# Optimization experiments

Hardware: AMD Instinct MI355X
Metric: run time of the kernel (lower is better)

## Reference

```python
import jax, jax.numpy as jnp
import numpy as np

B, S, D, M = 2, 4096, 128, 64

def _linear_init(key, shape, fan_in):
    bound = 1.0 / np.sqrt(fan_in)
    return jax.random.uniform(key, shape, jnp.float32, -bound, bound)

def setup_inputs() -> dict:
    key = jax.random.key(0)
    ks = jax.random.split(key, 18)
    x = jax.random.normal(ks[0], (B, S, D), jnp.float32)
    context = jax.random.normal(ks[1], (B, S, D), jnp.float32)
    # per-mechanism params (torch Linear semantics: y = x @ W.T + b)
    Wt = _linear_init(ks[2], (M, D, D), D)   # transform weight, laid out [m, in, out]
    bt = _linear_init(ks[3], (M, D), D)
    char = jax.random.normal(ks[4], (M, D), jnp.float32)  # characteristics [1,1,d] per mech
    Wg = _linear_init(ks[5], (M, D), D)      # timing_gate weight (out=1)
    bg = _linear_init(ks[6], (M,), D)
    Wv = _linear_init(ks[7], (M, D), D)      # victory_detector weight (out=1)
    bv = _linear_init(ks[8], (M,), D)
    O = jax.random.normal(ks[9], (M, M), jnp.float32) * 0.02  # overcoming matrix
    # selector: Linear(2D,2D) -> GELU -> Linear(2D,M)
    W1 = _linear_init(ks[10], (2 * D, 2 * D), 2 * D)
    b1 = _linear_init(ks[11], (2 * D,), 2 * D)
    W2 = _linear_init(ks[12], (2 * D, M), 2 * D)
    b2 = _linear_init(ks[13], (M,), 2 * D)
    # integrate: Linear(2D, D)
    Wi = _linear_init(ks[14], (2 * D, D), 2 * D)
    bi = _linear_init(ks[15], (D,), 2 * D)
    return {"x": x, "context": context, "Wt": Wt, "bt": bt, "char": char,
            "Wg": Wg, "bg": bg, "Wv": Wv, "bv": bv, "O": O,
            "W1": W1, "b1": b1, "W2": W2, "b2": b2, "Wi": Wi, "bi": bi}

def reference(x, context, Wt, bt, char, Wg, bg, Wv, bv, O, W1, b1, W2, b2, Wi, bi):
    # selection scores over mechanisms
    sel_in = jnp.concatenate([x, context], axis=-1)          # [b,s,2d]
    h = jax.nn.gelu(sel_in @ W1 + b1, approximate=False)
    selection_scores = jax.nn.softmax(h @ W2 + b2, axis=-1)  # [b,s,m]
    # all 64 mechanism nodes as one batched GEMM
    transformed = jnp.einsum('bsd,mde->bsme', x, Wt) + bt + char   # [b,s,m,d]
    timing = jax.nn.sigmoid(jnp.einsum('bsd,md->bsm', x, Wg) + bg)  # [b,s,m]
    victory = jax.nn.sigmoid(jnp.einsum('bsme,me->bsm', transformed, Wv) + bv)
    outputs = transformed * timing[..., None]                # [b,s,m,d]
    # strategic overcoming modulation: gate = 1 + tanh(scores @ O)
    gates = 1.0 + jnp.tanh(selection_scores @ O)             # [b,s,m]
    selected = jnp.einsum('bsme,bsm->bse', outputs, gates * selection_scores)
    victory_potential = jnp.sum(victory * selection_scores, axis=-1)  # [b,s]
    integrated = jnp.concatenate([x, selected], axis=-1) @ Wi + bi    # [b,s,d]
    return integrated, victory_potential
```

## Files before the change

kernel.cpp:

```cpp
#include <hip/hip_runtime.h>
#include <hip/hip_bf16.h>


typedef __bf16 bf16_t;
typedef __bf16 bf16x8 __attribute__((ext_vector_type(8)));
typedef float  f32x4  __attribute__((ext_vector_type(4)));

#define WS_WTT      0u
#define WS_W1T      2097152u
#define WS_W2T      2228224u
#define WS_OT       2260992u
#define WS_WG       2269184u
#define WS_U        2285568u
#define WS_CVEC     2301952u
#define WS_BCT      2302208u
#define WS_WIT      2318592u
#define WS_W        2384128u
#define WS_SBIAS    4481280u
#define WS_SEL      8675584u

#define VP_OFF 1048576

__device__ __forceinline__ f32x4 mfma16(bf16x8 a, bf16x8 b, f32x4 c) {
  return __builtin_amdgcn_mfma_f32_16x16x32_bf16(a, b, c, 0, 0, 0);
}

__device__ __forceinline__ void gld_lds16(const void* g, void* l) {
  __builtin_amdgcn_global_load_lds(
      (const __attribute__((address_space(1))) void*)g,
      (__attribute__((address_space(3))) void*)l, 16, 0, 0);
}

__device__ __forceinline__ float gelu_exact(float v) {
  return 0.5f * v * (1.0f + erff(v * 0.70710678118654752f));
}
__device__ __forceinline__ float sigmoidf_(float v) {
  return 1.0f / (1.0f + __expf(-v));
}

__global__ __launch_bounds__(256) void kprep(
    const float* __restrict__ Wt, const float* __restrict__ bt,
    const float* __restrict__ ch, const float* __restrict__ Wg,
    const float* __restrict__ Wv, const float* __restrict__ bv,
    const float* __restrict__ O, const float* __restrict__ W1,
    const float* __restrict__ W2, const float* __restrict__ Wi,
    char* __restrict__ ws)
{
  const int bid = blockIdx.x, tid = threadIdx.x;
  if (bid < 64) {
    const int m = bid;
    const float* wtm = Wt + m * 16384;
    bf16_t* wtt = (bf16_t*)(ws + WS_WTT) + m * 16384;
    #pragma unroll
    for (int i = 0; i < 8; ++i) {
      int task = tid + i * 256;
      int d = task >> 4, e0 = (task & 15) * 8;
      float vv[8];
      #pragma unroll
      for (int j = 0; j < 8; ++j) vv[j] = wtm[d * 128 + e0 + j];
      #pragma unroll
      for (int j = 0; j < 8; ++j) {
        int e = e0 + j;
        int q = e * 16 + (d >> 3);
        ((bf16_t*)((char*)wtt + ((q ^ (e & 7)) << 4)))[d & 7] = (bf16_t)vv[j];
      }
    }
    if (tid < 128) {
      const float* wvm = Wv + m * 128;
      float s = 0.f;
      for (int e = 0; e < 128; ++e) s += wtm[tid * 128 + e] * wvm[e];
      ((bf16_t*)(ws + WS_U))[m * 128 + tid] = (bf16_t)s;
    } else if (tid == 128) {
      const float* wvm = Wv + m * 128;
      float s = bv[m];
      for (int e = 0; e < 128; ++e) s += (bt[m * 128 + e] + ch[m * 128 + e]) * wvm[e];
      ((float*)(ws + WS_CVEC))[m] = s;
    }
  } else if (bid < 80) {
    int base = (bid - 64) * 256 + tid;
    int k = base >> 4, c0 = (base & 15) * 16;
    bf16_t* o = (bf16_t*)(ws + WS_W1T);
    #pragma unroll
    for (int j = 0; j < 16; ++j) o[(c0 + j) * 256 + k] = (bf16_t)W1[k * 256 + c0 + j];
  } else if (bid < 82) {
    int base = (bid - 80) * 256 + tid;
    int k = base >> 1, c0 = (base & 1) * 32;
    bf16_t* o = (bf16_t*)(ws + WS_W2T);
    #pragma unroll
    for (int j = 0; j < 32; ++j) o[(c0 + j) * 256 + k] = (bf16_t)W2[k * 64 + c0 + j];
  } else if (bid == 82) {
    int k = tid >> 2, c0 = (tid & 3) * 16;
    bf16_t* o = (bf16_t*)(ws + WS_OT);
    #pragma unroll
    for (int j = 0; j < 16; ++j) o[(c0 + j) * 64 + k] = (bf16_t)O[k * 64 + c0 + j];
  } else if (bid == 83) {
    bf16_t* o = (bf16_t*)(ws + WS_WG);
    #pragma unroll
    for (int j = 0; j < 32; ++j) o[tid * 32 + j] = (bf16_t)Wg[tid * 32 + j];
  } else if (bid == 84) {
    bf16_t* o = (bf16_t*)(ws + WS_BCT);
    #pragma unroll
    for (int i = 0; i < 4; ++i) {
      int task = tid + i * 256;
      int m = task >> 4, e0 = (task & 15) * 8;
      #pragma unroll
      for (int j = 0; j < 8; ++j)
        o[(e0 + j) * 64 + m] = (bf16_t)(bt[m * 128 + e0 + j] + ch[m * 128 + e0 + j]);
    }
  } else {
    int base = (bid - 85) * 256 + tid;
    int k = base >> 2, c0 = (base & 3) * 32;
    bf16_t* o = (bf16_t*)(ws + WS_WIT);
    #pragma unroll
    for (int j = 0; j < 32; ++j) o[(c0 + j) * 256 + k] = (bf16_t)Wi[k * 128 + c0 + j];
  }
}

__global__ __launch_bounds__(256) void kselect(
    const float* __restrict__ x, const float* __restrict__ ctx,
    const float* __restrict__ b1, const float* __restrict__ b2,
    const float* __restrict__ bg,
    char* __restrict__ ws, float* __restrict__ out)
{
  __shared__ char sm[41472];
  bf16_t* hL      = (bf16_t*)sm;
  float*  logitsL = (float*)(sm + 16384);
  float*  scoresL = (float*)(sm + 24576);
  bf16_t* scbL    = (bf16_t*)(sm + 32768);
  bf16_t* wbL     = (bf16_t*)(sm + 36864);
  float*  vpL     = (float*)(sm + 40960);

  const int tid = threadIdx.x;
  const int lane = tid & 63, wid = tid >> 6;
  const int tb = blockIdx.x * 32;
  const int lr = lane & 15;
  const int lk = (lane >> 4) * 8;
  const int lj4 = (lane >> 4) * 4;

  const bf16_t* W1t = (const bf16_t*)(ws + WS_W1T);
  const bf16_t* W2t = (const bf16_t*)(ws + WS_W2T);
  const bf16_t* Ot  = (const bf16_t*)(ws + WS_OT);
  const bf16_t* Wgb = (const bf16_t*)(ws + WS_WG);
  const bf16_t* Ub  = (const bf16_t*)(ws + WS_U);
  const float*  cv  = (const float*)(ws + WS_CVEC);
  const bf16_t* bct = (const bf16_t*)(ws + WS_BCT);
  float* wOut  = (float*)(ws + WS_W);
  float* sbOut = (float*)(ws + WS_SBIAS);

  bf16x8 aSel[2][8];
  #pragma unroll
  for (int rg = 0; rg < 2; ++rg) {
    int t = tb + rg * 16 + lr;
    #pragma unroll
    for (int ks = 0; ks < 8; ++ks) {
      const float* src = (ks < 4) ? (x + t * 128 + ks * 32 + lk)
                                  : (ctx + t * 128 + (ks - 4) * 32 + lk);
      bf16x8 a;
      #pragma unroll
      for (int j = 0; j < 8; ++j) a[j] = (bf16_t)src[j];
      aSel[rg][ks] = a;
    }
  }

  #pragma unroll
  for (int cg = 0; cg < 4; ++cg) {
    int c = wid * 64 + cg * 16 + lr;
    f32x4 a0 = {0.f,0.f,0.f,0.f}, a1 = {0.f,0.f,0.f,0.f};
    #pragma unroll
    for (int ks = 0; ks < 8; ++ks) {
      bf16x8 b = *(const bf16x8*)(W1t + c * 256 + ks * 32 + lk);
      a0 = mfma16(aSel[0][ks], b, a0);
      a1 = mfma16(aSel[1][ks], b, a1);
    }
    float bb = b1[c];
    #pragma unroll
    for (int j = 0; j < 4; ++j) {
      int r0 = lj4 + j, r1 = 16 + lj4 + j;
      float v0 = gelu_exact(a0[j] + bb);
      float v1 = gelu_exact(a1[j] + bb);
      *(bf16_t*)((char*)hL + ((r0 * 512 + c * 2) ^ ((r0 & 7) << 4))) = (bf16_t)v0;
      *(bf16_t*)((char*)hL + ((r1 * 512 + c * 2) ^ ((r1 & 7) << 4))) = (bf16_t)v1;
    }
  }
  __syncthreads();

  {
    int c = wid * 16 + lr;
    f32x4 l0 = {0.f,0.f,0.f,0.f}, l1 = {0.f,0.f,0.f,0.f};
    #pragma unroll
    for (int ks = 0; ks < 8; ++ks) {
      int k0 = ks * 32 + lk;
      bf16x8 a0 = *(const bf16x8*)((char*)hL + ((lr * 512 + k0 * 2) ^ ((lr & 7) << 4)));
      bf16x8 a1 = *(const bf16x8*)((char*)hL + (((16 + lr) * 512 + k0 * 2) ^ ((lr & 7) << 4)));
      bf16x8 b  = *(const bf16x8*)(W2t + c * 256 + k0);
      l0 = mfma16(a0, b, l0);
      l1 = mfma16(a1, b, l1);
    }
    float bb = b2[c];
    #pragma unroll
    for (int j = 0; j < 4; ++j) {
      logitsL[(lj4 + j) * 64 + c] = l0[j] + bb;
      logitsL[(16 + lj4 + j) * 64 + c] = l1[j] + bb;
    }
  }
  __syncthreads();

  {
    int row = tid >> 3, i = tid & 7;
    float v[8];
    #pragma unroll
    for (int j = 0; j < 8; ++j) v[j] = logitsL[row * 64 + i * 8 + j];
    float mx = v[0];
    #pragma unroll
    for (int j = 1; j < 8; ++j) mx = fmaxf(mx, v[j]);
    mx = fmaxf(mx, __shfl_xor(mx, 1));
    mx = fmaxf(mx, __shfl_xor(mx, 2));
    mx = fmaxf(mx, __shfl_xor(mx, 4));
    float sum = 0.f;
    #pragma unroll
    for (int j = 0; j < 8; ++j) { v[j] = __expf(v[j] - mx); sum += v[j]; }
    sum += __shfl_xor(sum, 1);
    sum += __shfl_xor(sum, 2);
    sum += __shfl_xor(sum, 4);
    float inv = 1.0f / sum;
    #pragma unroll
    for (int j = 0; j < 8; ++j) {
      float s = v[j] * inv;
      int cc = i * 8 + j;
      scoresL[row * 64 + cc] = s;
      *(bf16_t*)((char*)scbL + ((row * 128 + cc * 2) ^ ((row & 7) << 4))) = (bf16_t)s;
    }
  }
  __syncthreads();

  const int c = wid * 16 + lr;
  f32x4 g0 = {0.f,0.f,0.f,0.f}, g1 = {0.f,0.f,0.f,0.f};
  #pragma unroll
  for (int ks = 0; ks < 2; ++ks) {
    int k0 = ks * 32 + lk;
    bf16x8 a0 = *(const bf16x8*)((char*)scbL + ((lr * 128 + k0 * 2) ^ ((lr & 7) << 4)));
    bf16x8 a1 = *(const bf16x8*)((char*)scbL + (((16 + lr) * 128 + k0 * 2) ^ ((lr & 7) << 4)));
    bf16x8 b  = *(const bf16x8*)(Ot + c * 64 + k0);
    g0 = mfma16(a0, b, g0);
    g1 = mfma16(a1, b, g1);
  }
  f32x4 t0 = {0.f,0.f,0.f,0.f}, t1 = {0.f,0.f,0.f,0.f};
  f32x4 v0 = {0.f,0.f,0.f,0.f}, v1 = {0.f,0.f,0.f,0.f};
  #pragma unroll
  for (int ks = 0; ks < 4; ++ks) {
    bf16x8 bT = *(const bf16x8*)(Wgb + c * 128 + ks * 32 + lk);
    bf16x8 bV = *(const bf16x8*)(Ub  + c * 128 + ks * 32 + lk);
    t0 = mfma16(aSel[0][ks], bT, t0);
    t1 = mfma16(aSel[1][ks], bT, t1);
    v0 = mfma16(aSel[0][ks], bV, v0);
    v1 = mfma16(aSel[1][ks], bV, v1);
  }
  {
    float bgc = bg[c], cvc = cv[c];
    #pragma unroll
    for (int j = 0; j < 4; ++j) {
      {
        int r = lj4 + j;
        float gate = 1.0f + tanhf(g0[j]);
        float tim  = sigmoidf_(t0[j] + bgc);
        float vic  = sigmoidf_(v0[j] + cvc);
        float sc   = scoresL[r * 64 + c];
        float w    = gate * sc * tim;
        wOut[(tb + r) * 64 + c] = w;
        *(bf16_t*)((char*)wbL + ((r * 128 + c * 2) ^ ((r & 7) << 4))) = (bf16_t)w;
        float pv = vic * sc;
        pv += __shfl_xor(pv, 1); pv += __shfl_xor(pv, 2);
        pv += __shfl_xor(pv, 4); pv += __shfl_xor(pv, 8);
        if (lr == 0) vpL[r * 4 + wid] = pv;
      }
      {
        int r = 16 + lj4 + j;
        float gate = 1.0f + tanhf(g1[j]);
        float tim  = sigmoidf_(t1[j] + bgc);
        float vic  = sigmoidf_(v1[j] + cvc);
        float sc   = scoresL[r * 64 + c];
        float w    = gate * sc * tim;
        wOut[(tb + r) * 64 + c] = w;
        *(bf16_t*)((char*)wbL + ((r * 128 + c * 2) ^ ((r & 7) << 4))) = (bf16_t)w;
        float pv = vic * sc;
        pv += __shfl_xor(pv, 1); pv += __shfl_xor(pv, 2);
        pv += __shfl_xor(pv, 4); pv += __shfl_xor(pv, 8);
        if (lr == 0) vpL[r * 4 + wid] = pv;
      }
    }
  }
  __syncthreads();

  {
    f32x4 s00 = {0.f,0.f,0.f,0.f}, s01 = {0.f,0.f,0.f,0.f};
    f32x4 s10 = {0.f,0.f,0.f,0.f}, s11 = {0.f,0.f,0.f,0.f};
    int c0 = wid * 32 + lr, c1 = wid * 32 + 16 + lr;
    #pragma unroll
    for (int ks = 0; ks < 2; ++ks) {
      int k0 = ks * 32 + lk;
      bf16x8 a0 = *(const bf16x8*)((char*)wbL + ((lr * 128 + k0 * 2) ^ ((lr & 7) << 4)));
      bf16x8 a1 = *(const bf16x8*)((char*)wbL + (((16 + lr) * 128 + k0 * 2) ^ ((lr & 7) << 4)));
      bf16x8 bb0 = *(const bf16x8*)(bct + c0 * 64 + k0);
      bf16x8 bb1 = *(const bf16x8*)(bct + c1 * 64 + k0);
      s00 = mfma16(a0, bb0, s00); s01 = mfma16(a0, bb1, s01);
      s10 = mfma16(a1, bb0, s10); s11 = mfma16(a1, bb1, s11);
    }
    #pragma unroll
    for (int j = 0; j < 4; ++j) {
      sbOut[(tb + lj4 + j) * 128 + c0] = s00[j];
      sbOut[(tb + lj4 + j) * 128 + c1] = s01[j];
      sbOut[(tb + 16 + lj4 + j) * 128 + c0] = s10[j];
      sbOut[(tb + 16 + lj4 + j) * 128 + c1] = s11[j];
    }
  }
  if (tid < 32) {
    float s = vpL[tid * 4 + 0] + vpL[tid * 4 + 1] + vpL[tid * 4 + 2] + vpL[tid * 4 + 3];
    out[VP_OFF + tb + tid] = s;
  }
}

__global__ __launch_bounds__(256) void kmech(
    const float* __restrict__ x, char* __restrict__ ws)
{
  __shared__ char sm[49152];
  const int tid = threadIdx.x;
  const int lane = tid & 63, wid = tid >> 6;
  const int tb = (blockIdx.x >> 1) * 64;
  const int eh = blockIdx.x & 1;
  const int lr = lane & 15;
  const int lk = (lane >> 4) * 8;
  const int lj4 = (lane >> 4) * 4;
  const int wrow = (wid & 1) * 32;
  const int wcol = (wid >> 1) * 32;

  const char* wttAll = (const char*)(ws + WS_WTT);
  const float* wIn  = (const float*)(ws + WS_W);
  const float* sbIn = (const float*)(ws + WS_SBIAS);
  float* selOut = (float*)(ws + WS_SEL);
  float* wL = (float*)(sm + 32768);

  {
    const char* g = wttAll + 0 * 32768 + eh * 16384;
    char* l = sm + 0;
    #pragma unroll
    for (int r = 0; r < 4; ++r)
      gld_lds16(g + r * 4096 + tid * 16, l + r * 4096 + wid * 1024);
  }
  {
    const float4* s = (const float4*)(wIn + tb * 64);
    float4* d = (float4*)wL;
    #pragma unroll
    for (int i = 0; i < 4; ++i) d[tid + i * 256] = s[tid + i * 256];
  }
  bf16x8 aX[2][4];
  #pragma unroll
  for (int rg = 0; rg < 2; ++rg) {
    const float* xr = x + (tb + wrow + rg * 16 + lr) * 128;
    #pragma unroll
    for (int ks = 0; ks < 4; ++ks) {
      bf16x8 a;
      #pragma unroll
      for (int j = 0; j < 8; ++j) a[j] = (bf16_t)xr[ks * 32 + lk + j];
      aX[rg][ks] = a;
    }
  }
  f32x4 acc[2][2];
  #pragma unroll
  for (int rg = 0; rg < 2; ++rg)
    #pragma unroll
    for (int cg = 0; cg < 2; ++cg) {
      f32x4 a;
      #pragma unroll
      for (int j = 0; j < 4; ++j)
        a[j] = sbIn[(tb + wrow + rg * 16 + lj4 + j) * 128 + eh * 64 + wcol + cg * 16 + lr];
      acc[rg][cg] = a;
    }
  __syncthreads();

  const int e0 = wcol + lr, e1 = wcol + 16 + lr;
  for (int m = 0; m < 64; ++m) {
    const char* cur = sm + (m & 1) * 16384;
    if (m < 63) {
      const char* g = wttAll + (m + 1) * 32768 + eh * 16384;
      char* l = sm + ((m + 1) & 1) * 16384;
      #pragma unroll
      for (int r = 0; r < 4; ++r)
        gld_lds16(g + r * 4096 + tid * 16, l + r * 4096 + wid * 1024);
    }
    f32x4 y00 = {0.f,0.f,0.f,0.f}, y01 = {0.f,0.f,0.f,0.f};
    f32x4 y10 = {0.f,0.f,0.f,0.f}, y11 = {0.f,0.f,0.f,0.f};
    #pragma unroll
    for (int ks = 0; ks < 4; ++ks) {
      int u = (ks * 32 + lk) >> 3;
      bf16x8 b0 = *(const bf16x8*)(cur + (((e0 * 16 + u) ^ (e0 & 7)) << 4));
      bf16x8 b1 = *(const bf16x8*)(cur + (((e1 * 16 + u) ^ (e1 & 7)) << 4));
      y00 = mfma16(aX[0][ks], b0, y00);
      y01 = mfma16(aX[0][ks], b1, y01);
      y10 = mfma16(aX[1][ks], b0, y10);
      y11 = mfma16(aX[1][ks], b1, y11);
    }
    #pragma unroll
    for (int j = 0; j < 4; ++j) {
      float w0 = wL[(wrow + lj4 + j) * 64 + m];
      float w1 = wL[(wrow + 16 + lj4 + j) * 64 + m];
      acc[0][0][j] += w0 * y00[j];
      acc[0][1][j] += w0 * y01[j];
      acc[1][0][j] += w1 * y10[j];
      acc[1][1][j] += w1 * y11[j];
    }
    __syncthreads();
  }
  #pragma unroll
  for (int rg = 0; rg < 2; ++rg)
    #pragma unroll
    for (int cg = 0; cg < 2; ++cg)
      #pragma unroll
      for (int j = 0; j < 4; ++j)
        selOut[(tb + wrow + rg * 16 + lj4 + j) * 128 + eh * 64 + wcol + cg * 16 + lr]
            = acc[rg][cg][j];
}

__global__ __launch_bounds__(256) void kinteg(
    const float* __restrict__ x, const float* __restrict__ bi,
    const char* __restrict__ ws, float* __restrict__ out)
{
  const int tid = threadIdx.x;
  const int lane = tid & 63, wid = tid >> 6;
  const int tb = blockIdx.x * 32;
  const int lr = lane & 15, lk = (lane >> 4) * 8, lj4 = (lane >> 4) * 4;
  const bf16_t* Wit = (const bf16_t*)(ws + WS_WIT);
  const float* sel = (const float*)(ws + WS_SEL);

  bf16x8 aF[2][8];
  #pragma unroll
  for (int rg = 0; rg < 2; ++rg) {
    int t = tb + rg * 16 + lr;
    #pragma unroll
    for (int ks = 0; ks < 8; ++ks) {
      const float* src = (ks < 4) ? (x + t * 128 + ks * 32 + lk)
                                  : (sel + t * 128 + (ks - 4) * 32 + lk);
      bf16x8 a;
      #pragma unroll
      for (int j = 0; j < 8; ++j) a[j] = (bf16_t)src[j];
      aF[rg][ks] = a;
    }
  }
  #pragma unroll
  for (int cg = 0; cg < 2; ++cg) {
    int c = wid * 32 + cg * 16 + lr;
    f32x4 a0 = {0.f,0.f,0.f,0.f}, a1 = {0.f,0.f,0.f,0.f};
    #pragma unroll
    for (int ks = 0; ks < 8; ++ks) {
      bf16x8 b = *(const bf16x8*)(Wit + c * 256 + ks * 32 + lk);
      a0 = mfma16(aF[0][ks], b, a0);
      a1 = mfma16(aF[1][ks], b, a1);
    }
    float bb = bi[c];
    #pragma unroll
    for (int j = 0; j < 4; ++j) {
      out[(tb + lj4 + j) * 128 + c] = a0[j] + bb;
      out[(tb + 16 + lj4 + j) * 128 + c] = a1[j] + bb;
    }
  }
}

extern "C" void kernel_launch(void* const* d_in, const int* in_sizes, int n_in,
                              void* d_out, int out_size, void* d_ws, size_t ws_size,
                              hipStream_t stream)
{
  (void)in_sizes; (void)n_in; (void)out_size; (void)ws_size;
  const float* x   = (const float*)d_in[0];
  const float* ctx = (const float*)d_in[1];
  const float* Wt  = (const float*)d_in[2];
  const float* bt  = (const float*)d_in[3];
  const float* ch  = (const float*)d_in[4];
  const float* Wg  = (const float*)d_in[5];
  const float* bg  = (const float*)d_in[6];
  const float* Wv  = (const float*)d_in[7];
  const float* bv  = (const float*)d_in[8];
  const float* O   = (const float*)d_in[9];
  const float* W1  = (const float*)d_in[10];
  const float* b1  = (const float*)d_in[11];
  const float* W2  = (const float*)d_in[12];
  const float* b2  = (const float*)d_in[13];
  const float* Wi  = (const float*)d_in[14];
  const float* bi  = (const float*)d_in[15];
  float* out = (float*)d_out;
  char* ws = (char*)d_ws;

  kprep<<<89, 256, 0, stream>>>(Wt, bt, ch, Wg, Wv, bv, O, W1, W2, Wi, ws);
  kselect<<<256, 256, 0, stream>>>(x, ctx, b1, b2, bg, ws, out);
  kmech<<<256, 256, 0, stream>>>(x, ws);
  kinteg<<<256, 256, 0, stream>>>(x, bi, ws, out);
}
```

Before: 166.5 us.

## Stream mechanism weights directly into registers with multi-stage prefetch in kmech

New measurement: 143.8 us. 13.6% less time.

```diff
diff --git a/kernel.cpp b/kernel.cpp
--- a/kernel.cpp
+++ b/kernel.cpp
@@ -25,17 +25,18 @@
   return __builtin_amdgcn_mfma_f32_16x16x32_bf16(a, b, c, 0, 0, 0);
 }
 
-__device__ __forceinline__ void gld_lds16(const void* g, void* l) {
-  __builtin_amdgcn_global_load_lds(
-      (const __attribute__((address_space(1))) void*)g,
-      (__attribute__((address_space(3))) void*)l, 16, 0, 0);
-}
-
 __device__ __forceinline__ float gelu_exact(float v) {
   return 0.5f * v * (1.0f + erff(v * 0.70710678118654752f));
 }
 __device__ __forceinline__ float sigmoidf_(float v) {
   return 1.0f / (1.0f + __expf(-v));
+}
+
+__device__ __forceinline__ bf16x8 cvt8(float4 v0, float4 v1) {
+  bf16x8 a;
+  a[0] = (bf16_t)v0.x; a[1] = (bf16_t)v0.y; a[2] = (bf16_t)v0.z; a[3] = (bf16_t)v0.w;
+  a[4] = (bf16_t)v1.x; a[5] = (bf16_t)v1.y; a[6] = (bf16_t)v1.z; a[7] = (bf16_t)v1.w;
+  return a;
 }
 
 __global__ __launch_bounds__(256) void kprep(
@@ -47,57 +48,54 @@
     char* __restrict__ ws)
 {
   const int bid = blockIdx.x, tid = threadIdx.x;
-  if (bid < 64) {
-    const int m = bid;
+  if (bid < 128) {
+    const int m = bid >> 1, half = bid & 1;
     const float* wtm = Wt + m * 16384;
     bf16_t* wtt = (bf16_t*)(ws + WS_WTT) + m * 16384;
-    #pragma unroll
-    for (int i = 0; i < 8; ++i) {
-      int task = tid + i * 256;
-      int d = task >> 4, e0 = (task & 15) * 8;
-      float vv[8];
-      #pragma unroll
-      for (int j = 0; j < 8; ++j) vv[j] = wtm[d * 128 + e0 + j];
-      #pragma unroll
-      for (int j = 0; j < 8; ++j) {
-        int e = e0 + j;
-        int q = e * 16 + (d >> 3);
-        ((bf16_t*)((char*)wtt + ((q ^ (e & 7)) << 4)))[d & 7] = (bf16_t)vv[j];
+    const int ks = half * 2 + (tid >> 7), e = tid & 127;
+    bf16_t tmp[32];
+    #pragma unroll
+    for (int dd = 0; dd < 32; ++dd)
+      tmp[dd] = (bf16_t)wtm[(ks * 32 + dd) * 128 + e];
+    bf16_t* dst = wtt + ks * 4096 + e * 32;
+    #pragma unroll
+    for (int g = 0; g < 4; ++g)
+      *(bf16x8*)(dst + g * 8) = *(const bf16x8*)(tmp + g * 8);
+    if (half == 0) {
+      if (tid < 128) {
+        const float* wvm = Wv + m * 128;
+        float s = 0.f;
+        for (int e2 = 0; e2 < 128; ++e2) s += wtm[tid * 128 + e2] * wvm[e2];
+        ((bf16_t*)(ws + WS_U))[m * 128 + tid] = (bf16_t)s;
+      } else if (tid == 128) {
+        const float* wvm = Wv + m * 128;
+        float s = bv[m];
+        for (int e2 = 0; e2 < 128; ++e2) s += (bt[m * 128 + e2] + ch[m * 128 + e2]) * wvm[e2];
+        ((float*)(ws + WS_CVEC))[m] = s;
       }
     }
-    if (tid < 128) {
-      const float* wvm = Wv + m * 128;
-      float s = 0.f;
-      for (int e = 0; e < 128; ++e) s += wtm[tid * 128 + e] * wvm[e];
-      ((bf16_t*)(ws + WS_U))[m * 128 + tid] = (bf16_t)s;
-    } else if (tid == 128) {
-      const float* wvm = Wv + m * 128;
-      float s = bv[m];
-      for (int e = 0; e < 128; ++e) s += (bt[m * 128 + e] + ch[m * 128 + e]) * wvm[e];
-      ((float*)(ws + WS_CVEC))[m] = s;
-    }
-  } else if (bid < 80) {
-    int base = (bid - 64) * 256 + tid;
+  } else if (bid < 144) {
+    int base = (bid - 128) * 256 + tid;
     int k = base >> 4, c0 = (base & 15) * 16;
     bf16_t* o = (bf16_t*)(ws + WS_W1T);
     #pragma unroll
     for (int j = 0; j < 16; ++j) o[(c0 + j) * 256 + k] = (bf16_t)W1[k * 256 + c0 + j];
-  } else if (bid < 82) {
-    int base = (bid - 80) * 256 + tid;
+  } else if (bid < 146) {
+    int base = (bid - 144) * 256 + tid;
     int k = base >> 1, c0 = (base & 1) * 32;
     bf16_t* o = (bf16_t*)(ws + WS_W2T);
     #pragma unroll
     for (int j = 0; j < 32; ++j) o[(c0 + j) * 256 + k] = (bf16_t)W2[k * 64 + c0 + j];
-  } else if (bid == 82) {
+  } else if (bid == 146) {
     int k = tid >> 2, c0 = (tid & 3) * 16;
     bf16_t* o = (bf16_t*)(ws + WS_OT);
     #pragma unroll
     for (int j = 0; j < 16; ++j) o[(c0 + j) * 64 + k] = (bf16_t)O[k * 64 + c0 + j];
-  } else if (bid == 83) {
+  } else if (bid == 147) {
     bf16_t* o = (bf16_t*)(ws + WS_WG);
     #pragma unroll
     for (int j = 0; j < 32; ++j) o[tid * 32 + j] = (bf16_t)Wg[tid * 32 + j];
-  } else if (bid == 84) {
+  } else if (bid == 148) {
     bf16_t* o = (bf16_t*)(ws + WS_BCT);
     #pragma unroll
     for (int i = 0; i < 4; ++i) {
@@ -108,7 +106,7 @@
         o[(e0 + j) * 64 + m] = (bf16_t)(bt[m * 128 + e0 + j] + ch[m * 128 + e0 + j]);
     }
   } else {
-    int base = (bid - 85) * 256 + tid;
+    int base = (bid - 149) * 256 + tid;
     int k = base >> 2, c0 = (base & 3) * 32;
     bf16_t* o = (bf16_t*)(ws + WS_WIT);
     #pragma unroll
@@ -155,10 +153,7 @@
     for (int ks = 0; ks < 8; ++ks) {
       const float* src = (ks < 4) ? (x + t * 128 + ks * 32 + lk)
                                   : (ctx + t * 128 + (ks - 4) * 32 + lk);
-      bf16x8 a;
-      #pragma unroll
-      for (int j = 0; j < 8; ++j) a[j] = (bf16_t)src[j];
-      aSel[rg][ks] = a;
+      aSel[rg][ks] = cvt8(*(const float4*)src, *(const float4*)(src + 4));
     }
   }
 
@@ -319,105 +314,105 @@
   }
 }
 
-__global__ __launch_bounds__(256) void kmech(
+__device__ __forceinline__ void loadF(bf16x8 (&F)[4], const char* bbase, int m) {
+  const char* p = bbase + m * 32768;
+  F[0] = *(const bf16x8*)(p);
+  F[1] = *(const bf16x8*)(p + 8192);
+  F[2] = *(const bf16x8*)(p + 16384);
+  F[3] = *(const bf16x8*)(p + 24576);
+}
+
+template<int J>
+__device__ __forceinline__ void computeT(const bf16x8 (&F)[4], const f32x4 (&wc)[16],
+                                         const bf16x8 (&aX)[4][4], f32x4 (&acc)[4]) {
+  #pragma unroll
+  for (int rg = 0; rg < 4; ++rg) {
+    f32x4 y = {0.f, 0.f, 0.f, 0.f};
+    #pragma unroll
+    for (int ks = 0; ks < 4; ++ks) y = mfma16(aX[rg][ks], F[ks], y);
+    #pragma unroll
+    for (int jj = 0; jj < 4; ++jj)
+      acc[rg][jj] += wc[rg * 4 + jj][J] * y[jj];
+  }
+}
+
+__global__ __launch_bounds__(256, 1) void kmech(
     const float* __restrict__ x, char* __restrict__ ws)
 {
-  __shared__ char sm[49152];
+  __shared__ float wL[64 * 64];
   const int tid = threadIdx.x;
   const int lane = tid & 63, wid = tid >> 6;
   const int tb = (blockIdx.x >> 1) * 64;
   const int eh = blockIdx.x & 1;
-  const int lr = lane & 15;
-  const int lk = (lane >> 4) * 8;
-  const int lj4 = (lane >> 4) * 4;
-  const int wrow = (wid & 1) * 32;
-  const int wcol = (wid >> 1) * 32;
-
-  const char* wttAll = (const char*)(ws + WS_WTT);
+  const int lr = lane & 15, lg = lane >> 4;
+  const int lj4 = lg * 4;
+  const int wcol = wid * 16;
+
+  const char* wttc = (const char*)(ws + WS_WTT);
   const float* wIn  = (const float*)(ws + WS_W);
   const float* sbIn = (const float*)(ws + WS_SBIAS);
   float* selOut = (float*)(ws + WS_SEL);
-  float* wL = (float*)(sm + 32768);
-
-  {
-    const char* g = wttAll + 0 * 32768 + eh * 16384;
-    char* l = sm + 0;
-    #pragma unroll
-    for (int r = 0; r < 4; ++r)
-      gld_lds16(g + r * 4096 + tid * 16, l + r * 4096 + wid * 1024);
-  }
+
   {
     const float4* s = (const float4*)(wIn + tb * 64);
     float4* d = (float4*)wL;
     #pragma unroll
     for (int i = 0; i < 4; ++i) d[tid + i * 256] = s[tid + i * 256];
   }
-  bf16x8 aX[2][4];
-  #pragma unroll
-  for (int rg = 0; rg < 2; ++rg) {
-    const float* xr = x + (tb + wrow + rg * 16 + lr) * 128;
-    #pragma unroll
-    for (int ks = 0; ks < 4; ++ks) {
-      bf16x8 a;
+  bf16x8 aX[4][4];
+  #pragma unroll
+  for (int rg = 0; rg < 4; ++rg) {
+    const float* xr = x + (tb + rg * 16 + lr) * 128;
+    #pragma unroll
+    for (int ks = 0; ks < 4; ++ks)
+      aX[rg][ks] = cvt8(*(const float4*)(xr + ks * 32 + lg * 8),
+                        *(const float4*)(xr + ks * 32 + lg * 8 + 4));
+  }
+  f32x4 acc[4];
+  #pragma unroll
+  for (int rg = 0; rg < 4; ++rg) {
+    f32x4 a;
+    #pragma unroll
+    for (int j = 0; j < 4; ++j)
+      a[j] = sbIn[(tb + rg * 16 + lj4 + j) * 128 + eh * 64 + wcol + lr];
+    acc[rg] = a;
+  }
+  __syncthreads();
+
+  const char* bbase = wttc + (size_t)(((eh * 64 + wcol + lr) * 32 + lg * 8) * 2);
+
+  bf16x8 F0[4], F1[4], F2[4], F3[4];
+  loadF(F0, bbase, 0);
+  loadF(F1, bbase, 1);
+  loadF(F2, bbase, 2);
+
+  for (int it = 0; it < 16; ++it) {
+    const int base = it * 4;
+    f32x4 wc[16];
+    #pragma unroll
+    for (int rg = 0; rg < 4; ++rg)
       #pragma unroll
-      for (int j = 0; j < 8; ++j) a[j] = (bf16_t)xr[ks * 32 + lk + j];
-      aX[rg][ks] = a;
-    }
-  }
-  f32x4 acc[2][2];
-  #pragma unroll
-  for (int rg = 0; rg < 2; ++rg)
-    #pragma unroll
-    for (int cg = 0; cg < 2; ++cg) {
-      f32x4 a;
-      #pragma unroll
-      for (int j = 0; j < 4; ++j)
-        a[j] = sbIn[(tb + wrow + rg * 16 + lj4 + j) * 128 + eh * 64 + wcol + cg * 16 + lr];
-      acc[rg][cg] = a;
-    }
-  __syncthreads();
-
-  const int e0 = wcol + lr, e1 = wcol + 16 + lr;
-  for (int m = 0; m < 64; ++m) {
-    const char* cur = sm + (m & 1) * 16384;
-    if (m < 63) {
-      const char* g = wttAll + (m + 1) * 32768 + eh * 16384;
-      char* l = sm + ((m + 1) & 1) * 16384;
-      #pragma unroll
-      for (int r = 0; r < 4; ++r)
-        gld_lds16(g + r * 4096 + tid * 16, l + r * 4096 + wid * 1024);
-    }
-    f32x4 y00 = {0.f,0.f,0.f,0.f}, y01 = {0.f,0.f,0.f,0.f};
-    f32x4 y10 = {0.f,0.f,0.f,0.f}, y11 = {0.f,0.f,0.f,0.f};
-    #pragma unroll
-    for (int ks = 0; ks < 4; ++ks) {
-      int u = (ks * 32 + lk) >> 3;
-      bf16x8 b0 = *(const bf16x8*)(cur + (((e0 * 16 + u) ^ (e0 & 7)) << 4));
-      bf16x8 b1 = *(const bf16x8*)(cur + (((e1 * 16 + u) ^ (e1 & 7)) << 4));
-      y00 = mfma16(aX[0][ks], b0, y00);
-      y01 = mfma16(aX[0][ks], b1, y01);
-      y10 = mfma16(aX[1][ks], b0, y10);
-      y11 = mfma16(aX[1][ks], b1, y11);
-    }
-    #pragma unroll
-    for (int j = 0; j < 4; ++j) {
-      float w0 = wL[(wrow + lj4 + j) * 64 + m];
-      float w1 = wL[(wrow + 16 + lj4 + j) * 64 + m];
-      acc[0][0][j] += w0 * y00[j];
-      acc[0][1][j] += w0 * y01[j];
-      acc[1][0][j] += w1 * y10[j];
-      acc[1][1][j] += w1 * y11[j];
-    }
-    __syncthreads();
-  }
-  #pragma unroll
-  for (int rg = 0; rg < 2; ++rg)
-    #pragma unroll
-    for (int cg = 0; cg < 2; ++cg)
-      #pragma unroll
-      for (int j = 0; j < 4; ++j)
-        selOut[(tb + wrow + rg * 16 + lj4 + j) * 128 + eh * 64 + wcol + cg * 16 + lr]
-            = acc[rg][cg][j];
+      for (int jj = 0; jj < 4; ++jj)
+        wc[rg * 4 + jj] = *(const f32x4*)(&wL[(rg * 16 + lj4 + jj) * 64 + base]);
+    int n3 = base + 3;
+    int n4 = base + 4 > 63 ? 63 : base + 4;
+    int n5 = base + 5 > 63 ? 63 : base + 5;
+    int n6 = base + 6 > 63 ? 63 : base + 6;
+    loadF(F3, bbase, n3);
+    computeT<0>(F0, wc, aX, acc);
+    loadF(F0, bbase, n4);
+    computeT<1>(F1, wc, aX, acc);
+    loadF(F1, bbase, n5);
+    computeT<2>(F2, wc, aX, acc);
+    loadF(F2, bbase, n6);
+    computeT<3>(F3, wc, aX, acc);
+  }
+
+  #pragma unroll
+  for (int rg = 0; rg < 4; ++rg)
+    #pragma unroll
+    for (int j = 0; j < 4; ++j)
+      selOut[(tb + rg * 16 + lj4 + j) * 128 + eh * 64 + wcol + lr] = acc[rg][j];
 }
 
 __global__ __launch_bounds__(256) void kinteg(
@@ -439,10 +434,7 @@
     for (int ks = 0; ks < 8; ++ks) {
       const float* src = (ks < 4) ? (x + t * 128 + ks * 32 + lk)
                                   : (sel + t * 128 + (ks - 4) * 32 + lk);
-      bf16x8 a;
-      #pragma unroll
-      for (int j = 0; j < 8; ++j) a[j] = (bf16_t)src[j];
-      aF[rg][ks] = a;
+      aF[rg][ks] = cvt8(*(const float4*)src, *(const float4*)(src + 4));
     }
   }
   #pragma unroll
@@ -488,7 +480,7 @@
   float* out = (float*)d_out;
   char* ws = (char*)d_ws;
 
-  kprep<<<89, 256, 0, stream>>>(Wt, bt, ch, Wg, Wv, bv, O, W1, W2, Wi, ws);
+  kprep<<<153, 256, 0, stream>>>(Wt, bt, ch, Wg, Wv, bv, O, W1, W2, Wi, ws);
   kselect<<<256, 256, 0, stream>>>(x, ctx, b1, b2, bg, ws, out);
   kmech<<<256, 256, 0, stream>>>(x, ws);
   kinteg<<<256, 256, 0, stream>>>(x, bi, ws, out);
```
